# Kernel tuning notes

Measured on AMD Instinct MI355X. Metric: run time of the kernel, lower is better.

## Reference

```python
import jax, jax.numpy as jnp
import numpy as np
import math

B, S, D, H, R, DFF = 4, 1024, 1024, 16, 64, 4096

def _layernorm(x, g, b, eps=1e-5):
    m = jnp.mean(x, axis=-1, keepdims=True)
    v = jnp.var(x, axis=-1, keepdims=True)
    return (x - m) / jnp.sqrt(v + eps) * g + b

def setup_inputs() -> dict:
    key = jax.random.key(0)
    ks = jax.random.split(key, 12)
    sc = 0.02
    return {
        "src": jax.random.normal(ks[0], (B, S, D), jnp.float32),
        "in_proj_w": jax.random.normal(ks[1], (3 * D, D), jnp.float32) * sc,
        "in_proj_b": jnp.zeros((3 * D,), jnp.float32),
        "out_proj_w": jax.random.normal(ks[2], (D, D), jnp.float32) * sc,
        "out_proj_b": jnp.zeros((D,), jnp.float32),
        "Qp_w": jax.random.normal(ks[3], (R, D), jnp.float32) * sc,
        "Qp_b": jnp.zeros((R,), jnp.float32),
        "Kp_w": jax.random.normal(ks[4], (R, D), jnp.float32) * sc,
        "Kp_b": jnp.zeros((R,), jnp.float32),
        "Vp_w": jax.random.normal(ks[5], (D, D), jnp.float32) * sc,
        "Vp_b": jnp.zeros((D,), jnp.float32),
        "lam": jnp.float32(0.5),
        "ff1_w": jax.random.normal(ks[6], (DFF, D), jnp.float32) * sc,
        "ff1_b": jnp.zeros((DFF,), jnp.float32),
        "ff2_w": jax.random.normal(ks[7], (D, DFF), jnp.float32) * sc,
        "ff2_b": jnp.zeros((D,), jnp.float32),
        "ln1_g": jnp.ones((D,), jnp.float32),
        "ln1_b": jnp.zeros((D,), jnp.float32),
        "ln2_g": jnp.ones((D,), jnp.float32),
        "ln2_b": jnp.zeros((D,), jnp.float32),
    }

def reference(src, in_proj_w, in_proj_b, out_proj_w, out_proj_b,
              Qp_w, Qp_b, Kp_w, Kp_b, Vp_w, Vp_b, lam,
              ff1_w, ff1_b, ff2_w, ff2_b, ln1_g, ln1_b, ln2_g, ln2_b):
    b, s, d = src.shape
    dh = d // H
    # ---- dense multi-head attention (torch nn.MultiheadAttention, eval) ----
    qkv = src @ in_proj_w.T + in_proj_b            # [B,S,3D]
    q, k, v = jnp.split(qkv, 3, axis=-1)
    q = q.reshape(b, s, H, dh).transpose(0, 2, 1, 3)  # [B,H,S,dh]
    k = k.reshape(b, s, H, dh).transpose(0, 2, 1, 3)
    v = v.reshape(b, s, H, dh).transpose(0, 2, 1, 3)
    scores = jnp.einsum('bhqd,bhkd->bhqk', q, k) / math.sqrt(dh)
    attn = jax.nn.softmax(scores, axis=-1)
    ctx = jnp.einsum('bhqk,bhkd->bhqd', attn, v)
    ctx = ctx.transpose(0, 2, 1, 3).reshape(b, s, d)
    dense_output = ctx @ out_proj_w.T + out_proj_b
    # ---- low-rank top-k sparse attention ----
    Q = src @ Qp_w.T + Qp_b                        # [B,S,R]
    K = src @ Kp_w.T + Kp_b
    V = src @ Vp_w.T + Vp_b                        # [B,S,D]
    QK = jnp.einsum('bqr,bkr->bqk', Q, K) / math.sqrt(R)
    aw = jax.nn.softmax(QK, axis=-1)               # [B,S,S]
    kk = max(1, int(s * 0.2))
    topv, topi = jax.lax.top_k(aw, kk)             # [B,S,kk]
    bi = jnp.arange(b)[:, None, None]
    si = jnp.arange(s)[None, :, None]
    sparse_attn = jnp.zeros_like(aw).at[bi, si, topi].set(topv)
    sparse_attn = sparse_attn / (jnp.sum(sparse_attn, axis=-1, keepdims=True) + 1e-9)
    sparse_output = jnp.einsum('bqk,bkd->bqd', sparse_attn, V)
    # ---- fuse, residual, norm, FFN ----
    sig = jax.nn.sigmoid(lam)
    fused = sig * dense_output + (1.0 - sig) * sparse_output
    x = _layernorm(src + fused, ln1_g, ln1_b)
    ff = jax.nn.relu(x @ ff1_w.T + ff1_b) @ ff2_w.T + ff2_b
    return _layernorm(x + ff, ln2_g, ln2_b)
```

## Files before the change

### kernel.cpp

```cpp
#include <hip/hip_runtime.h>
#include <hip/hip_bf16.h>
#include <math.h>

typedef __hip_bfloat16 bf16;
typedef __attribute__((ext_vector_type(8))) short short8;
typedef __attribute__((ext_vector_type(4))) float f32x4;

#define NB 4
#define NS 1024
#define ND 1024
#define NH 16
#define NDH 64
#define NR 64
#define NDFF 4096
#define NM (NB*NS)
#define NTOPK 204

static __device__ __forceinline__ float b2f(bf16 x) { return __bfloat162float(x); }
static __device__ __forceinline__ bf16  f2b(float x) { return __float2bfloat16(x); }
static __device__ __forceinline__ unsigned short bfbits(float x) {
  bf16 h = __float2bfloat16(x);
  return *reinterpret_cast<unsigned short*>(&h);
}

static __device__ __forceinline__ void gload_lds16(const void* g, void* l) {
  __builtin_amdgcn_global_load_lds(
      (const __attribute__((address_space(1))) void*)g,
      (__attribute__((address_space(3))) void*)l, 16, 0, 0);
}

static __device__ __forceinline__ void ld8(const bf16* p, float* d) {
  const uint4 u = *(const uint4*)p;
  d[0] = __uint_as_float((u.x & 0xffffu) << 16);
  d[1] = __uint_as_float(u.x & 0xffff0000u);
  d[2] = __uint_as_float((u.y & 0xffffu) << 16);
  d[3] = __uint_as_float(u.y & 0xffff0000u);
  d[4] = __uint_as_float((u.z & 0xffffu) << 16);
  d[5] = __uint_as_float(u.z & 0xffff0000u);
  d[6] = __uint_as_float((u.w & 0xffffu) << 16);
  d[7] = __uint_as_float(u.w & 0xffff0000u);
}

static __device__ __forceinline__ float block_sum_256(float v, float* rbuf, int tid) {
  rbuf[tid] = v;
  __syncthreads();
  #pragma unroll
  for (int st = 128; st > 0; st >>= 1) {
    if (tid < st) rbuf[tid] += rbuf[tid + st];
    __syncthreads();
  }
  const float r = rbuf[0];
  __syncthreads();
  return r;
}

__global__ __launch_bounds__(256) void cast_kernel(const float* __restrict__ in,
                                                   bf16* __restrict__ out, int n) {
  const int i = (blockIdx.x * 256 + threadIdx.x) * 4;
  if (i < n) {
    const float4 v = *(const float4*)(in + i);
    uint2 o;
    o.x = (unsigned)bfbits(v.x) | ((unsigned)bfbits(v.y) << 16);
    o.y = (unsigned)bfbits(v.z) | ((unsigned)bfbits(v.w) << 16);
    *(uint2*)(out + i) = o;
  }
}

__global__ __launch_bounds__(256) void pack_qk_kernel(
    const float* __restrict__ Qw, const float* __restrict__ Kw,
    const float* __restrict__ Qb, const float* __restrict__ Kb,
    bf16* __restrict__ w, float* __restrict__ bias) {
  const int r = blockIdx.x;
  const float* srcw = (r < 64) ? (Qw + (size_t)r * ND) : (Kw + (size_t)(r - 64) * ND);
  for (int i = threadIdx.x; i < ND; i += 256) w[(size_t)r * ND + i] = f2b(srcw[i]);
  if (r == 0)
    for (int i = threadIdx.x; i < 128; i += 256)
      bias[i] = (i < 64) ? Qb[i] : Kb[i - 64];
}

template<int BM, int BN, int BK, int BIAS, int RELU, int OUTF32>
__global__ __launch_bounds__(256) void mfma_gemm(
    const bf16* __restrict__ A, const bf16* __restrict__ W,
    const float* __restrict__ bias, void* __restrict__ C,
    int K, int lda, int ldb, int ldc,
    long long aHi, long long aLo, long long bHi, long long bLo,
    long long cHi, long long cLo, float scale)
{
  constexpr int WTM = BM / 2;
  constexpr int WTN = BN / 2;
  constexpr int AM = WTM / 16;
  constexpr int AN = WTN / 16;
  constexpr int KK = BK / 32;
  constexpr int SLOTS = BK / 8;
  constexpr int RPC = 512 / BK;
  __shared__ short As[2][BM * BK];
  __shared__ short Bs[2][BN * BK];
  const int tid  = threadIdx.x;
  const int lane = tid & 63;
  const int w    = tid >> 6;
  const int z    = blockIdx.z;
  const long long aOff = (long long)(z >> 4) * aHi + (long long)(z & 15) * aLo;
  const long long bOff = (long long)(z >> 4) * bHi + (long long)(z & 15) * bLo;
  const long long cOff = (long long)(z >> 4) * cHi + (long long)(z & 15) * cLo;

  int bx = blockIdx.x, by = blockIdx.y;
  if ((gridDim.x & 7) == 0) {
    const unsigned lin = blockIdx.y * gridDim.x + blockIdx.x;
    const unsigned Wd = gridDim.x >> 3;
    const unsigned xcd = lin & 7, i = lin >> 3;
    bx = (int)(xcd * Wd + (i % Wd));
    by = (int)(i / Wd);
  }
  const int m0 = by * BM;
  const int n0 = bx * BN;
  const int wr = w >> 1, wc = w & 1;
  const int lm = lane & 15, quad = lane >> 4;

  f32x4 acc[AM][AN];
  #pragma unroll
  for (int i = 0; i < AM; ++i)
    #pragma unroll
    for (int j = 0; j < AN; ++j) acc[i][j] = (f32x4){0.f, 0.f, 0.f, 0.f};

  const int slot = lane & (SLOTS - 1);
  const int sr   = lane / SLOTS;
  const int swz  = (BK == 32) ? ((sr >> 1) & 3) : (sr & 7);
  const int scol = (slot ^ swz) << 3;
  const int xv   = (BK == 32) ? ((lm >> 1) & 3) : (lm & 7);
  const bf16* Ab = A + aOff;
  const bf16* Bb = W + bOff;

  auto stage = [&](int buf, int k0) {
    #pragma unroll
    for (int t = 0; t < (BM * BK) / 2048; ++t) {
      const int row = w * (BM / 4) + t * RPC;
      gload_lds16(Ab + (long long)(m0 + row + sr) * lda + k0 + scol, &As[buf][row * BK]);
    }
    #pragma unroll
    for (int t = 0; t < (BN * BK) / 2048; ++t) {
      const int row = w * (BN / 4) + t * RPC;
      gload_lds16(Bb + (long long)(n0 + row + sr) * ldb + k0 + scol, &Bs[buf][row * BK]);
    }
  };
  auto compute = [&](int buf) {
    #pragma unroll
    for (int kk = 0; kk < KK; ++kk) {
      const int cb = ((kk * 4 + quad) ^ xv) << 3;
      short8 af[AM], bfr[AN];
      #pragma unroll
      for (int i = 0; i < AM; ++i)
        af[i] = *(const short8*)&As[buf][(wr * WTM + i * 16 + lm) * BK + cb];
      #pragma unroll
      for (int j = 0; j < AN; ++j)
        bfr[j] = *(const short8*)&Bs[buf][(wc * WTN + j * 16 + lm) * BK + cb];
      #pragma unroll
      for (int i = 0; i < AM; ++i)
        #pragma unroll
        for (int j = 0; j < AN; ++j)
          acc[i][j] = __builtin_amdgcn_mfma_f32_16x16x32_bf16(af[i], bfr[j], acc[i][j], 0, 0, 0);
    }
  };

  stage(0, 0);
  __syncthreads();
  int cur = 0;
  for (int k0 = BK; k0 < K; k0 += BK) {
    stage(cur ^ 1, k0);
    compute(cur);
    __syncthreads();
    cur ^= 1;
  }
  compute(cur);

  #pragma unroll
  for (int i = 0; i < AM; ++i) {
    #pragma unroll
    for (int j = 0; j < AN; ++j) {
      const int n = n0 + wc * WTN + j * 16 + lm;
      const float bj = BIAS ? bias[n] : 0.f;
      #pragma unroll
      for (int rr = 0; rr < 4; ++rr) {
        const int m = m0 + wr * WTM + i * 16 + quad * 4 + rr;
        float v = acc[i][j][rr] * scale + bj;
        if (RELU) v = fmaxf(v, 0.f);
        const long long co = cOff + (long long)m * ldc + n;
        if (OUTF32) ((float*)C)[co] = v;
        else        ((bf16*)C)[co] = f2b(v);
      }
    }
  }
}

__global__ __launch_bounds__(256) void attn_kernel(
    const bf16* __restrict__ qkv,
    const bf16* __restrict__ Vt,
    bf16* __restrict__ ctx)
{
  __shared__ short smem[2][2][64 * 64];
  const int tid = threadIdx.x, lane = tid & 63, w = tid >> 6;
  const int lm = lane & 15, quad = lane >> 4;
  const int z = blockIdx.y, b = z >> 4, h = z & 15;
  const int q0 = blockIdx.x * 128;
  const bf16* Qb = qkv + (long long)b * NS * 3072 + h * 64;
  const bf16* Kb = Qb + ND;
  const bf16* Vb = Vt + (long long)z * (NDH * NS);

  short8 qf[2][2];
  #pragma unroll
  for (int j = 0; j < 2; ++j)
    #pragma unroll
    for (int kk = 0; kk < 2; ++kk)
      qf[j][kk] = *(const short8*)(Qb + (long long)(q0 + w * 32 + j * 16 + lm) * 3072
                                      + kk * 32 + quad * 8);

  const int slot = lane & 7, sr = lane >> 3;
  const int scol = (slot ^ sr) << 3;

  auto stage = [&](int buf, int t) {
    #pragma unroll
    for (int u = 0; u < 2; ++u) {
      const int row = w * 16 + u * 8;
      gload_lds16(Kb + (long long)(t * 64 + row + sr) * 3072 + scol,
                  &smem[buf][0][row * 64]);
    }
    #pragma unroll
    for (int u = 0; u < 2; ++u) {
      const int row = w * 16 + u * 8;
      gload_lds16(Vb + (long long)(row + sr) * NS + t * 64 + scol,
                  &smem[buf][1][row * 64]);
    }
  };

  f32x4 o[4][2];
  #pragma unroll
  for (int i = 0; i < 4; ++i)
    #pragma unroll
    for (int j = 0; j < 2; ++j) o[i][j] = (f32x4){0.f, 0.f, 0.f, 0.f};
  float m[2] = {-1e30f, -1e30f}, l[2] = {0.f, 0.f};

  stage(0, 0);
  __syncthreads();
  for (int t = 0; t < 16; ++t) {
    const int buf = t & 1;
    if (t < 15) stage(buf ^ 1, t + 1);

    f32x4 st[4][2];
    #pragma unroll
    for (int i = 0; i < 4; ++i)
      #pragma unroll
      for (int j = 0; j < 2; ++j) st[i][j] = (f32x4){0.f, 0.f, 0.f, 0.f};
    #pragma unroll
    for (int kk = 0; kk < 2; ++kk) {
      const int cb = ((kk * 4 + quad) ^ (lm & 7)) << 3;
      short8 ka[4];
      #pragma unroll
      for (int i = 0; i < 4; ++i)
        ka[i] = *(const short8*)&smem[buf][0][(i * 16 + lm) * 64 + cb];
      #pragma unroll
      for (int i = 0; i < 4; ++i)
        #pragma unroll
        for (int j = 0; j < 2; ++j)
          st[i][j] = __builtin_amdgcn_mfma_f32_16x16x32_bf16(ka[i], qf[j][kk], st[i][j], 0, 0, 0);
    }

    #pragma unroll
    for (int j = 0; j < 2; ++j) {
      float pm = -1e30f;
      #pragma unroll
      for (int i = 0; i < 4; ++i)
        #pragma unroll
        for (int r = 0; r < 4; ++r) {
          st[i][j][r] *= 0.125f;
          pm = fmaxf(pm, st[i][j][r]);
        }
      pm = fmaxf(pm, __shfl_xor(pm, 16, 64));
      pm = fmaxf(pm, __shfl_xor(pm, 32, 64));
      const float mn = fmaxf(m[j], pm);
      const float sc = __expf(m[j] - mn);
      float ps = 0.f;
      #pragma unroll
      for (int i = 0; i < 4; ++i)
        #pragma unroll
        for (int r = 0; r < 4; ++r) {
          const float e = __expf(st[i][j][r] - mn);
          st[i][j][r] = e;
          ps += e;
        }
      ps += __shfl_xor(ps, 16, 64);
      ps += __shfl_xor(ps, 32, 64);
      l[j] = l[j] * sc + ps;
      m[j] = mn;
      #pragma unroll
      for (int i = 0; i < 4; ++i)
        #pragma unroll
        for (int r = 0; r < 4; ++r) o[i][j][r] *= sc;
    }

    unsigned u0[4][2], u1[4][2];
    #pragma unroll
    for (int i = 0; i < 4; ++i)
      #pragma unroll
      for (int j = 0; j < 2; ++j) {
        u0[i][j] = (unsigned)bfbits(st[i][j][0]) | ((unsigned)bfbits(st[i][j][1]) << 16);
        u1[i][j] = (unsigned)bfbits(st[i][j][2]) | ((unsigned)bfbits(st[i][j][3]) << 16);
      }
    const int s0l = ((quad & 1) * 2) * 16 + lm;
    const int s1l = s0l + 16;
    const bool hi = (quad >> 1) != 0;

    #pragma unroll
    for (int kk = 0; kk < 2; ++kk) {
      short8 pf[2];
      #pragma unroll
      for (int j = 0; j < 2; ++j) {
        const unsigned a0 = __shfl(u0[kk * 2][j],     s0l, 64);
        const unsigned a1 = __shfl(u1[kk * 2][j],     s0l, 64);
        const unsigned b0 = __shfl(u0[kk * 2 + 1][j], s0l, 64);
        const unsigned b1 = __shfl(u1[kk * 2 + 1][j], s0l, 64);
        const unsigned c0 = __shfl(u0[kk * 2][j],     s1l, 64);
        const unsigned c1 = __shfl(u1[kk * 2][j],     s1l, 64);
        const unsigned d0 = __shfl(u0[kk * 2 + 1][j], s1l, 64);
        const unsigned d1 = __shfl(u1[kk * 2 + 1][j], s1l, 64);
        union { uint4 u; short8 s; } cv;
        cv.u.x = hi ? b0 : a0; cv.u.y = hi ? b1 : a1;
        cv.u.z = hi ? d0 : c0; cv.u.w = hi ? d1 : c1;
        pf[j] = cv.s;
      }
      const int cb = ((kk * 4 + quad) ^ (lm & 7)) << 3;
      short8 va[4];
      #pragma unroll
      for (int i = 0; i < 4; ++i)
        va[i] = *(const short8*)&smem[buf][1][(i * 16 + lm) * 64 + cb];
      #pragma unroll
      for (int i = 0; i < 4; ++i)
        #pragma unroll
        for (int j = 0; j < 2; ++j)
          o[i][j] = __builtin_amdgcn_mfma_f32_16x16x32_bf16(va[i], pf[j], o[i][j], 0, 0, 0);
    }
    __syncthreads();
  }

  short (*OL)[72] = (short(*)[72])&smem[0][0][0];
  #pragma unroll
  for (int j = 0; j < 2; ++j) {
    const float inv = 1.f / l[j];
    #pragma unroll
    for (int i = 0; i < 4; ++i) {
      uint2 u;
      u.x = (unsigned)bfbits(o[i][j][0] * inv) | ((unsigned)bfbits(o[i][j][1] * inv) << 16);
      u.y = (unsigned)bfbits(o[i][j][2] * inv) | ((unsigned)bfbits(o[i][j][3] * inv) << 16);
      *(uint2*)&OL[w * 32 + j * 16 + lm][i * 16 + quad * 4] = u;
    }
  }
  __syncthreads();
  {
    const int q = tid >> 1, c = (tid & 1) * 32;
    const uint4 r0 = *(const uint4*)&OL[q][c];
    const uint4 r1 = *(const uint4*)&OL[q][c + 8];
    const uint4 r2 = *(const uint4*)&OL[q][c + 16];
    const uint4 r3 = *(const uint4*)&OL[q][c + 24];
    bf16* dst = ctx + ((long long)(b * NS + q0 + q)) * 1024 + h * 64 + c;
    ((uint4*)dst)[0] = r0; ((uint4*)dst)[1] = r1;
    ((uint4*)dst)[2] = r2; ((uint4*)dst)[3] = r3;
  }
}

__global__ __launch_bounds__(256) void transpose_v_kernel(
    const bf16* __restrict__ qkv, bf16* __restrict__ Vt) {
  __shared__ short T[64][72];
  const int tid = threadIdx.x;
  const int h = blockIdx.y;
  const int b = blockIdx.z;
  const int s0 = blockIdx.x * 64;
  const bf16* src = qkv + ((long long)b * NS + s0) * 3072 + 2 * ND + h * 64;
  {
    const int s = tid >> 2, c = (tid & 3) * 16;
    const uint4 a0 = *(const uint4*)(src + (long long)s * 3072 + c);
    const uint4 a1 = *(const uint4*)(src + (long long)s * 3072 + c + 8);
    *(uint4*)&T[s][c] = a0; *(uint4*)&T[s][c + 8] = a1;
  }
  __syncthreads();
  {
    const int d = tid >> 2, c = (tid & 3) * 16;
    unsigned wds[8];
    #pragma unroll
    for (int u = 0; u < 8; ++u) {
      const unsigned lo = (unsigned short)T[c + 2 * u][d];
      const unsigned hi = (unsigned short)T[c + 2 * u + 1][d];
      wds[u] = lo | (hi << 16);
    }
    bf16* dst = Vt + (long long)(b * NH + h) * (NDH * NS) + (long long)d * NS + s0 + c;
    uint4 o0, o1;
    o0.x = wds[0]; o0.y = wds[1]; o0.z = wds[2]; o0.w = wds[3];
    o1.x = wds[4]; o1.y = wds[5]; o1.z = wds[6]; o1.w = wds[7];
    ((uint4*)dst)[0] = o0; ((uint4*)dst)[1] = o1;
  }
}

__global__ __launch_bounds__(256) void transpose_sq_kernel(
    const bf16* __restrict__ src, bf16* __restrict__ dst) {
  __shared__ short T[64][72];
  const int tid = threadIdx.x;
  const int b = blockIdx.z;
  const int s0 = blockIdx.x * 64, d0 = blockIdx.y * 64;
  const bf16* sp = src + ((long long)b * NS + s0) * ND + d0;
  {
    const int s = tid >> 2, c = (tid & 3) * 16;
    const uint4 a0 = *(const uint4*)(sp + (long long)s * ND + c);
    const uint4 a1 = *(const uint4*)(sp + (long long)s * ND + c + 8);
    *(uint4*)&T[s][c] = a0; *(uint4*)&T[s][c + 8] = a1;
  }
  __syncthreads();
  {
    const int d = tid >> 2, c = (tid & 3) * 16;
    unsigned wds[8];
    #pragma unroll
    for (int u = 0; u < 8; ++u) {
      const unsigned lo = (unsigned short)T[c + 2 * u][d];
      const unsigned hi = (unsigned short)T[c + 2 * u + 1][d];
      wds[u] = lo | (hi << 16);
    }
    bf16* dp = dst + ((long long)b * ND + d0 + d) * NS + s0 + c;
    uint4 o0, o1;
    o0.x = wds[0]; o0.y = wds[1]; o0.z = wds[2]; o0.w = wds[3];
    o1.x = wds[4]; o1.y = wds[5]; o1.z = wds[6]; o1.w = wds[7];
    ((uint4*)dp)[0] = o0; ((uint4*)dp)[1] = o1;
  }
}

__global__ __launch_bounds__(256) void sparse_select_kernel(
    const float* __restrict__ S, bf16* __restrict__ aw)
{
  __shared__ unsigned hist[4][256];
  const int tid = threadIdx.x;
  const int lane = tid & 63;
  const int wv = tid >> 6;
  const long long row = (long long)blockIdx.x * 4 + wv;

  float sv[16];
  const float* sp = S + row * 1024 + lane * 16;
  #pragma unroll
  for (int c = 0; c < 4; ++c) {
    const float4 v = ((const float4*)sp)[c];
    sv[4*c] = v.x; sv[4*c+1] = v.y; sv[4*c+2] = v.z; sv[4*c+3] = v.w;
  }
  unsigned key[16];
  #pragma unroll
  for (int j = 0; j < 16; ++j) {
    const unsigned u = __float_as_uint(sv[j]);
    key[j] = (u & 0x80000000u) ? ~u : (u | 0x80000000u);
  }

  unsigned pref = 0u;
  int need = NTOPK;
  #pragma unroll
  for (int p = 3; p >= 0; --p) {
    *(uint4*)&hist[wv][lane * 4] = (uint4){0u, 0u, 0u, 0u};
    __syncthreads();
    const int sh = (p + 1) * 8;
    #pragma unroll
    for (int j = 0; j < 16; ++j) {
      const bool part = (p == 3) || ((key[j] >> sh) == pref);
      if (part) atomicAdd(&hist[wv][(key[j] >> (p * 8)) & 255u], 1u);
    }
    __syncthreads();
    const unsigned h0 = hist[wv][4*lane],     h1 = hist[wv][4*lane + 1];
    const unsigned h2 = hist[wv][4*lane + 2], h3 = hist[wv][4*lane + 3];
    const unsigned s3 = h3, s2 = h2 + s3, s1 = h1 + s2, s0 = h0 + s1;
    unsigned sum = s0;
    #pragma unroll
    for (int d2 = 1; d2 < 64; d2 <<= 1) {
      const unsigned t = __shfl_down(sum, d2, 64);
      if (lane < 64 - d2) sum += t;
    }
    const unsigned above = sum - s0;
    const unsigned cum[4]  = {above + s0, above + s1, above + s2, above + s3};
    const unsigned next[4] = {above + s1, above + s2, above + s3, above};
    unsigned candPref = 0u; int candNeed = 0; bool has = false;
    #pragma unroll
    for (int i = 0; i < 4; ++i) {
      if ((int)cum[i] >= need && (int)next[i] < need) {
        has = true;
        candPref = (pref << 8) | (unsigned)(4 * lane + i);
        candNeed = need - (int)next[i];
      }
    }
    const unsigned long long m = __ballot(has);
    const int srcLane = (int)(__ffsll((long long)m) - 1);
    pref = (unsigned)__shfl((int)candPref, srcLane, 64);
    need = __shfl(candNeed, srcLane, 64);
  }

  const unsigned T = pref;
  const unsigned tb = (T & 0x80000000u) ? (T ^ 0x80000000u) : ~T;
  const float thr = __uint_as_float(tb);

  float wvv[16];
  float psTop = 0.f, psAll = 0.f;
  #pragma unroll
  for (int j = 0; j < 16; ++j) {
    const float e = __expf(sv[j] - thr);
    psAll += e;
    const float wt = (key[j] >= T) ? e : 0.f;
    psTop += wt;
    wvv[j] = wt;
  }
  #pragma unroll
  for (int s = 1; s < 64; s <<= 1) {
    psTop += __shfl_xor(psTop, s, 64);
    psAll += __shfl_xor(psAll, s, 64);
  }
  const float inv = 1.f / (psTop + 1e-9f * psAll);

  uint4 o0, o1;
  o0.x = (unsigned)bfbits(wvv[0]*inv)  | ((unsigned)bfbits(wvv[1]*inv)  << 16);
  o0.y = (unsigned)bfbits(wvv[2]*inv)  | ((unsigned)bfbits(wvv[3]*inv)  << 16);
  o0.z = (unsigned)bfbits(wvv[4]*inv)  | ((unsigned)bfbits(wvv[5]*inv)  << 16);
  o0.w = (unsigned)bfbits(wvv[6]*inv)  | ((unsigned)bfbits(wvv[7]*inv)  << 16);
  o1.x = (unsigned)bfbits(wvv[8]*inv)  | ((unsigned)bfbits(wvv[9]*inv)  << 16);
  o1.y = (unsigned)bfbits(wvv[10]*inv) | ((unsigned)bfbits(wvv[11]*inv) << 16);
  o1.z = (unsigned)bfbits(wvv[12]*inv) | ((unsigned)bfbits(wvv[13]*inv) << 16);
  o1.w = (unsigned)bfbits(wvv[14]*inv) | ((unsigned)bfbits(wvv[15]*inv) << 16);
  bf16* op = aw + row * 1024 + lane * 16;
  ((uint4*)op)[0] = o0; ((uint4*)op)[1] = o1;
}

__global__ __launch_bounds__(256) void fuse_ln1_kernel(
    const float* __restrict__ src, const bf16* __restrict__ dense,
    const bf16* __restrict__ sparse, const float* __restrict__ lam,
    const float* __restrict__ g, const float* __restrict__ beta,
    bf16* __restrict__ x1)
{
  __shared__ float y[ND];
  __shared__ float rbuf[256];
  const int tid = threadIdx.x;
  const size_t base = (size_t)blockIdx.x * ND;
  const float sig = 1.f / (1.f + __expf(-lam[0]));
  const float c1 = 1.f - sig;
  float s1 = 0.f, s2 = 0.f;
  #pragma unroll
  for (int j = 0; j < 4; ++j) {
    const int i = tid + (j << 8);
    const float v = src[base + i] + sig * b2f(dense[base + i]) + c1 * b2f(sparse[base + i]);
    y[i] = v; s1 += v; s2 += v * v;
  }
  const float sum1 = block_sum_256(s1, rbuf, tid);
  const float sum2 = block_sum_256(s2, rbuf, tid);
  const float mean = sum1 * (1.f / ND);
  const float var  = sum2 * (1.f / ND) - mean * mean;
  const float rstd = rsqrtf(var + 1e-5f);
  #pragma unroll
  for (int j = 0; j < 4; ++j) {
    const int i = tid + (j << 8);
    x1[base + i] = f2b((y[i] - mean) * rstd * g[i] + beta[i]);
  }
}

__global__ __launch_bounds__(256) void ln2_kernel(
    const bf16* __restrict__ x1, const bf16* __restrict__ ff,
    const float* __restrict__ g, const float* __restrict__ beta,
    float* __restrict__ outp)
{
  __shared__ float y[ND];
  __shared__ float rbuf[256];
  const int tid = threadIdx.x;
  const size_t base = (size_t)blockIdx.x * ND;
  float s1 = 0.f, s2 = 0.f;
  #pragma unroll
  for (int j = 0; j < 4; ++j) {
    const int i = tid + (j << 8);
    const float v = b2f(x1[base + i]) + b2f(ff[base + i]);
    y[i] = v; s1 += v; s2 += v * v;
  }
  const float sum1 = block_sum_256(s1, rbuf, tid);
  const float sum2 = block_sum_256(s2, rbuf, tid);
  const float mean = sum1 * (1.f / ND);
  const float var  = sum2 * (1.f / ND) - mean * mean;
  const float rstd = rsqrtf(var + 1e-5f);
  #pragma unroll
  for (int j = 0; j < 4; ++j) {
    const int i = tid + (j << 8);
    outp[base + i] = (y[i] - mean) * rstd * g[i] + beta[i];
  }
}

extern "C" void kernel_launch(void* const* d_in, const int* in_sizes, int n_in,
                              void* d_out, int out_size, void* d_ws, size_t ws_size,
                              hipStream_t stream)
{
  const float* src        = (const float*)d_in[0];
  const float* in_proj_w  = (const float*)d_in[1];
  const float* in_proj_b  = (const float*)d_in[2];
  const float* out_proj_w = (const float*)d_in[3];
  const float* out_proj_b = (const float*)d_in[4];
  const float* Qp_w  = (const float*)d_in[5];
  const float* Qp_b  = (const float*)d_in[6];
  const float* Kp_w  = (const float*)d_in[7];
  const float* Kp_b  = (const float*)d_in[8];
  const float* Vp_w  = (const float*)d_in[9];
  const float* Vp_b  = (const float*)d_in[10];
  const float* lam   = (const float*)d_in[11];
  const float* ff1_w = (const float*)d_in[12];
  const float* ff1_b = (const float*)d_in[13];
  const float* ff2_w = (const float*)d_in[14];
  const float* ff2_b = (const float*)d_in[15];
  const float* ln1_g = (const float*)d_in[16];
  const float* ln1_b = (const float*)d_in[17];
  const float* ln2_g = (const float*)d_in[18];
  const float* ln2_b = (const float*)d_in[19];
  (void)in_sizes; (void)n_in; (void)out_size; (void)ws_size;

  char* ws = (char*)d_ws;
  size_t off = 0;
  auto take = [&](size_t bytes) -> void* {
    void* p = ws + off; off += (bytes + 255) & ~(size_t)255; return p;
  };
  bf16*  src_bf  = (bf16*) take((size_t)NM * ND * 2);
  bf16*  w_qkv   = (bf16*) take((size_t)3 * ND * ND * 2);
  bf16*  w_out   = (bf16*) take((size_t)ND * ND * 2);
  bf16*  w_vp    = (bf16*) take((size_t)ND * ND * 2);
  bf16*  w_ff1   = (bf16*) take((size_t)NDFF * ND * 2);
  bf16*  w_ff2   = (bf16*) take((size_t)ND * NDFF * 2);
  bf16*  w_qk    = (bf16*) take((size_t)128 * ND * 2);
  float* bias_qk = (float*)take(128 * 4);
  const size_t mark = off;
  bf16*  qkv     = (bf16*) take((size_t)NM * 3 * ND * 2);
  bf16*  Vt_all  = (bf16*) take((size_t)NH * NS * NS * 2);
  bf16*  Vt_old  = (bf16*) take((size_t)NH * NDH * NS * 2);
  bf16*  ctx     = (bf16*) take((size_t)NM * ND * 2);
  bf16*  dense   = (bf16*) take((size_t)NM * ND * 2);
  bf16*  QKs_bf  = (bf16*) take((size_t)NM * 128 * 2);
  bf16*  Vsp     = (bf16*) take((size_t)NM * ND * 2);
  bf16*  sparse  = (bf16*) take((size_t)NM * ND * 2);
  (void)Vt_old;
  bf16*  x1    = (bf16*)(ws + mark);
  bf16*  h1    = (bf16*)(ws + mark + (size_t)NM * ND * 2);
  bf16*  ffout = (bf16*)(ws + mark + (size_t)NM * ND * 2 + (size_t)NM * NDFF * 2);
  bf16*  aw    = (bf16*)(ws + mark + 2 * (size_t)NM * ND * 2 + (size_t)NM * NDFF * 2);
  float* S_sp  = (float*)(ws + mark + (size_t)NM * ND * 2);
  bf16*  Vsp_t = (bf16*)ctx;

  const dim3 blk(256);
  auto cast = [&](const float* in, bf16* out, int n) {
    cast_kernel<<<dim3((n + 1023) / 1024), blk, 0, stream>>>(in, out, n);
  };
  cast(src,        src_bf, NM * ND);
  cast(in_proj_w,  w_qkv,  3 * ND * ND);
  cast(out_proj_w, w_out,  ND * ND);
  cast(Vp_w,       w_vp,   ND * ND);
  cast(ff1_w,      w_ff1,  NDFF * ND);
  cast(ff2_w,      w_ff2,  ND * NDFF);
  pack_qk_kernel<<<dim3(128), blk, 0, stream>>>(Qp_w, Kp_w, Qp_b, Kp_b, w_qk, bias_qk);

  mfma_gemm<128,128,32,1,0,0><<<dim3(3*ND/128, NM/128, 1), blk, 0, stream>>>(
      src_bf, w_qkv, in_proj_b, qkv, ND, ND, ND, 3*ND, 0,0, 0,0, 0,0, 1.f);

  transpose_v_kernel<<<dim3(NS/64, NH, NB), blk, 0, stream>>>(qkv, Vt_all);
  attn_kernel<<<dim3(NS/128, NB*NH), blk, 0, stream>>>(qkv, Vt_all, ctx);

  mfma_gemm<128,64,64,1,0,0><<<dim3(ND/64, NM/128, 1), blk, 0, stream>>>(
      ctx, w_out, out_proj_b, dense, ND, ND, ND, ND, 0,0, 0,0, 0,0, 1.f);
  mfma_gemm<128,64,64,1,0,0><<<dim3(2, NM/128, 1), blk, 0, stream>>>(
      src_bf, w_qk, bias_qk, QKs_bf, ND, ND, ND, 128, 0,0, 0,0, 0,0, 1.f);
  mfma_gemm<128,64,64,0,0,1><<<dim3(NS/64, NS/128, NB), blk, 0, stream>>>(
      QKs_bf, QKs_bf + 64, nullptr, S_sp, 64, 128, 128, NS,
      0, (long long)NS*128, 0, (long long)NS*128, 0, (long long)NS*NS, 0.125f);
  mfma_gemm<128,64,64,1,0,0><<<dim3(ND/64, NM/128, 1), blk, 0, stream>>>(
      src_bf, w_vp, Vp_b, Vsp, ND, ND, ND, ND, 0,0, 0,0, 0,0, 1.f);
  transpose_sq_kernel<<<dim3(NS/64, ND/64, NB), blk, 0, stream>>>(Vsp, Vsp_t);
  sparse_select_kernel<<<dim3(NM/4), blk, 0, stream>>>(S_sp, aw);
  mfma_gemm<128,64,64,0,0,0><<<dim3(ND/64, NS/128, NB), blk, 0, stream>>>(
      aw, Vsp_t, nullptr, sparse, NS, NS, NS, ND,
      0, (long long)NS*ND, 0, (long long)ND*NS, 0, (long long)NS*ND, 1.f);
  fuse_ln1_kernel<<<dim3(NM), blk, 0, stream>>>(src, dense, sparse, lam, ln1_g, ln1_b, x1);
  mfma_gemm<128,128,32,1,1,0><<<dim3(NDFF/128, NM/128, 1), blk, 0, stream>>>(
      x1, w_ff1, ff1_b, h1, ND, ND, ND, NDFF, 0,0, 0,0, 0,0, 1.f);
  mfma_gemm<128,64,64,1,0,0><<<dim3(ND/64, NM/128, 1), blk, 0, stream>>>(
      h1, w_ff2, ff2_b, ffout, NDFF, NDFF, NDFF, ND, 0,0, 0,0, 0,0, 1.f);
  ln2_kernel<<<dim3(NM), blk, 0, stream>>>(x1, ffout, ln2_g, ln2_b, (float*)d_out);
}
```

Baseline: 463.7 us.

## Use partial vmcnt waits in GEMM/attention pipelines and merge six cast launches

In the GEMM and attention loops, the full __syncthreads after each stage is replaced by a partial s_waitcnt vmcnt plus a raw s_barrier. Waves now wait only for the previous tile's global-to-LDS loads while the next tile's loads stay in flight, so prefetch overlaps compute more. Separately, the six fp32-to-bf16 cast launches are merged into one kernel that picks its tensor from a block-range table, removing launch overhead. The risk is that the hand-written vmcnt counts must exactly match the number of loads issued per thread, or reads of unfinished LDS tiles will race.

```diff
diff --git a/kernel.cpp b/kernel.cpp
--- a/kernel.cpp
+++ b/kernel.cpp
@@ -27,6 +27,19 @@
   __builtin_amdgcn_global_load_lds(
       (const __attribute__((address_space(1))) void*)g,
       (__attribute__((address_space(3))) void*)l, 16, 0, 0);
+}
+
+template<int N> static __device__ __forceinline__ void vm_wait() {
+  if constexpr (N == 0)       asm volatile("s_waitcnt vmcnt(0)" ::: "memory");
+  else if constexpr (N == 2)  asm volatile("s_waitcnt vmcnt(2)" ::: "memory");
+  else if constexpr (N == 4)  asm volatile("s_waitcnt vmcnt(4)" ::: "memory");
+  else if constexpr (N == 6)  asm volatile("s_waitcnt vmcnt(6)" ::: "memory");
+  else if constexpr (N == 8)  asm volatile("s_waitcnt vmcnt(8)" ::: "memory");
+  else if constexpr (N == 12) asm volatile("s_waitcnt vmcnt(12)" ::: "memory");
+  else static_assert(N == 0, "unsupported vmcnt");
+}
+static __device__ __forceinline__ void bar() {
+  asm volatile("s_barrier" ::: "memory");
 }
 
 static __device__ __forceinline__ void ld8(const bf16* p, float* d) {
@@ -54,16 +67,25 @@
   return r;
 }
 
-__global__ __launch_bounds__(256) void cast_kernel(const float* __restrict__ in,
-                                                   bf16* __restrict__ out, int n) {
-  const int i = (blockIdx.x * 256 + threadIdx.x) * 4;
-  if (i < n) {
-    const float4 v = *(const float4*)(in + i);
-    uint2 o;
-    o.x = (unsigned)bfbits(v.x) | ((unsigned)bfbits(v.y) << 16);
-    o.y = (unsigned)bfbits(v.z) | ((unsigned)bfbits(v.w) << 16);
-    *(uint2*)(out + i) = o;
-  }
+struct CastArgs {
+  const float* in[6];
+  bf16* out[6];
+  unsigned end[6];
+};
+__global__ __launch_bounds__(256) void cast6_kernel(CastArgs a) {
+  const unsigned b = blockIdx.x;
+  int r = 0; unsigned base = 0;
+  #pragma unroll
+  for (int k = 0; k < 5; ++k)
+    if (b >= a.end[k]) { r = k + 1; base = a.end[k]; }
+  const float* in = a.in[r];
+  bf16* out = a.out[r];
+  const unsigned i = ((b - base) * 256 + threadIdx.x) * 4;
+  const float4 v = *(const float4*)(in + i);
+  uint2 o;
+  o.x = (unsigned)bfbits(v.x) | ((unsigned)bfbits(v.y) << 16);
+  o.y = (unsigned)bfbits(v.z) | ((unsigned)bfbits(v.w) << 16);
+  *(uint2*)(out + i) = o;
 }
 
 __global__ __launch_bounds__(256) void pack_qk_kernel(
@@ -93,6 +115,7 @@
   constexpr int KK = BK / 32;
   constexpr int SLOTS = BK / 8;
   constexpr int RPC = 512 / BK;
+  constexpr int LPW = (BM * BK) / 2048 + (BN * BK) / 2048;
   __shared__ short As[2][BM * BK];
   __shared__ short Bs[2][BN * BK];
   const int tid  = threadIdx.x;
@@ -162,14 +185,17 @@
   };
 
   stage(0, 0);
-  __syncthreads();
   int cur = 0;
   for (int k0 = BK; k0 < K; k0 += BK) {
     stage(cur ^ 1, k0);
+    vm_wait<LPW>();
+    bar();
     compute(cur);
-    __syncthreads();
+    bar();
     cur ^= 1;
   }
+  vm_wait<0>();
+  bar();
   compute(cur);
 
   #pragma unroll
@@ -239,10 +265,11 @@
   float m[2] = {-1e30f, -1e30f}, l[2] = {0.f, 0.f};
 
   stage(0, 0);
-  __syncthreads();
   for (int t = 0; t < 16; ++t) {
     const int buf = t & 1;
-    if (t < 15) stage(buf ^ 1, t + 1);
+    if (t < 15) { stage(buf ^ 1, t + 1); vm_wait<4>(); }
+    else        { vm_wait<0>(); }
+    bar();
 
     f32x4 st[4][2];
     #pragma unroll
@@ -337,7 +364,7 @@
         for (int j = 0; j < 2; ++j)
           o[i][j] = __builtin_amdgcn_mfma_f32_16x16x32_bf16(va[i], pf[j], o[i][j], 0, 0, 0);
     }
-    __syncthreads();
+    bar();
   }
 
   short (*OL)[72] = (short(*)[72])&smem[0][0][0];
@@ -641,15 +668,18 @@
   bf16*  Vsp_t = (bf16*)ctx;
 
   const dim3 blk(256);
-  auto cast = [&](const float* in, bf16* out, int n) {
-    cast_kernel<<<dim3((n + 1023) / 1024), blk, 0, stream>>>(in, out, n);
-  };
-  cast(src,        src_bf, NM * ND);
-  cast(in_proj_w,  w_qkv,  3 * ND * ND);
-  cast(out_proj_w, w_out,  ND * ND);
-  cast(Vp_w,       w_vp,   ND * ND);
-  cast(ff1_w,      w_ff1,  NDFF * ND);
-  cast(ff2_w,      w_ff2,  ND * NDFF);
+  {
+    CastArgs a;
+    a.in[0] = src;        a.out[0] = src_bf;
+    a.in[1] = in_proj_w;  a.out[1] = w_qkv;
+    a.in[2] = out_proj_w; a.out[2] = w_out;
+    a.in[3] = Vp_w;       a.out[3] = w_vp;
+    a.in[4] = ff1_w;      a.out[4] = w_ff1;
+    a.in[5] = ff2_w;      a.out[5] = w_ff2;
+    a.end[0] = 4096; a.end[1] = 7168; a.end[2] = 8192;
+    a.end[3] = 9216; a.end[4] = 13312; a.end[5] = 17408;
+    cast6_kernel<<<dim3(17408), blk, 0, stream>>>(a);
+  }
   pack_qk_kernel<<<dim3(128), blk, 0, stream>>>(Qp_w, Kp_w, Qp_b, Kp_b, w_qk, bias_qk);
 
   mfma_gemm<128,128,32,1,0,0><<<dim3(3*ND/128, NM/128, 1), blk, 0, stream>>>(
```

New measurement: 445.9 us. 3.8% less time.
